# Optimization experiments

Hardware: AMD Instinct MI355X
Metric: run time of the kernel (lower is better)

The kernel has to match this reference:

```python
import jax, jax.numpy as jnp
import numpy as np

B, S, H, DH = 2, 4096, 8, 64
D = H * DH  # 512

def setup_inputs() -> dict:
    key = jax.random.key(0)
    ks = jax.random.split(key, 9)
    sc = 1.0 / np.sqrt(D)
    return {
        "hidden_states": jax.random.normal(ks[0], (B, S, D), jnp.float32),
        "Wq": jax.random.normal(ks[1], (D, D), jnp.float32) * sc,
        "bq": jax.random.normal(ks[2], (D,), jnp.float32) * 0.02,
        "Wk": jax.random.normal(ks[3], (D, D), jnp.float32) * sc,
        "bk": jax.random.normal(ks[4], (D,), jnp.float32) * 0.02,
        "Wv": jax.random.normal(ks[5], (D, D), jnp.float32) * sc,
        "bv": jax.random.normal(ks[6], (D,), jnp.float32) * 0.02,
        "Wo": jax.random.normal(ks[7], (D, D), jnp.float32) * sc,
        "bo": jax.random.normal(ks[8], (D,), jnp.float32) * 0.02,
    }

def _split_heads(t):
    # (B, S, H*DH) -> (B, H, S, DH)
    b = t.shape[0]
    return t.reshape(b, S, H, DH).transpose(0, 2, 1, 3)

def reference(hidden_states, Wq, bq, Wk, bk, Wv, bv, Wo, bo):
    q = _split_heads(hidden_states @ Wq + bq)
    k = _split_heads(hidden_states @ Wk + bk)
    v = _split_heads(hidden_states @ Wv + bv)
    scale = 1.0 / jnp.sqrt(jnp.asarray(DH, q.dtype))
    energy = jnp.einsum('bhqd,bhkd->bhqk', q, k) * scale
    weights = jax.nn.softmax(energy, axis=-1)  # full O(S^2) matrix, as in source
    attended = jnp.einsum('bhqv,bhvd->bhqd', weights, v)
    merged = attended.transpose(0, 2, 1, 3).reshape(hidden_states.shape[0], S, D)
    return merged @ Wo + bo
```

## Files before the change

kernel.cpp:

```cpp
#include <hip/hip_runtime.h>
#include <cstdint>

typedef __bf16 bf16;
typedef __bf16 bf16x4 __attribute__((ext_vector_type(4)));
typedef __bf16 bf16x8 __attribute__((ext_vector_type(8)));
typedef float floatx4 __attribute__((ext_vector_type(4)));

#define MFMA32(a, b, c) __builtin_amdgcn_mfma_f32_16x16x32_bf16((a), (b), (c), 0, 0, 0)

__device__ inline bf16x8 cvt8(const float* p) {
    float4 u = *(const float4*)p;
    float4 v = *(const float4*)(p + 4);
    bf16x8 r;
    r[0] = (bf16)u.x; r[1] = (bf16)u.y; r[2] = (bf16)u.z; r[3] = (bf16)u.w;
    r[4] = (bf16)v.x; r[5] = (bf16)v.y; r[6] = (bf16)v.z; r[7] = (bf16)v.w;
    return r;
}

__global__ __launch_bounds__(256) void k_transpose(
    const float* __restrict__ w0, const float* __restrict__ w1,
    const float* __restrict__ w2, const float* __restrict__ w3,
    bf16* __restrict__ o0, bf16* __restrict__ o1,
    bf16* __restrict__ o2, bf16* __restrict__ o3)
{
    __shared__ float t[32][33];
    const float* in;
    bf16* out;
    switch (blockIdx.z) {
        case 0: in = w0; out = o0; break;
        case 1: in = w1; out = o1; break;
        case 2: in = w2; out = o2; break;
        default: in = w3; out = o3; break;
    }
    const int tx = threadIdx.x & 31;
    const int ty = threadIdx.x >> 5;
    const int r0 = blockIdx.y * 32;
    const int c0 = blockIdx.x * 32;
    #pragma unroll
    for (int i = 0; i < 32; i += 8)
        t[ty + i][tx] = in[(size_t)(r0 + ty + i) * 512 + c0 + tx];
    __syncthreads();
    #pragma unroll
    for (int i = 0; i < 32; i += 8)
        out[(size_t)(c0 + ty + i) * 512 + r0 + tx] = (bf16)t[tx][ty + i];
}

__global__ __launch_bounds__(256) void k_cvtx(
    const float* __restrict__ X, bf16* __restrict__ Xb)
{
    const size_t idx = ((size_t)blockIdx.x * 256 + threadIdx.x) * 8;
    *(bf16x8*)(Xb + idx) = cvt8(X + idx);
}

__global__ __launch_bounds__(256) void k_qkv(
    const bf16* __restrict__ Xb, const bf16* __restrict__ Wcat,
    const float* __restrict__ bq, const float* __restrict__ bk, const float* __restrict__ bv,
    bf16* __restrict__ Qs, bf16* __restrict__ Ks, bf16* __restrict__ Vt)
{
    __shared__ __align__(16) unsigned char smem[36864];
    uint4* Al = (uint4*)smem;
    uint4* Bl = (uint4*)(smem + 16384);

    const int tid  = threadIdx.x;
    const int w    = tid >> 6;
    const int lane = tid & 63;
    const int col  = lane & 15;
    const int quad = lane >> 4;
    const int m0 = blockIdx.x * 128;
    const int n0 = blockIdx.y * 128;

    const bf16* gA0 = Xb   + (size_t)(m0 + (tid >> 2)) * 512 + (tid & 3) * 8;
    const bf16* gA1 = gA0 + 64 * 512;
    const bf16* gB0 = Wcat + (size_t)(n0 + (tid >> 2)) * 512 + (tid & 3) * 8;
    const bf16* gB1 = gB0 + 64 * 512;

    const floatx4 zf = {0.f, 0.f, 0.f, 0.f};
    floatx4 acc[4][4];
    #pragma unroll
    for (int a = 0; a < 4; ++a)
        #pragma unroll
        for (int b = 0; b < 4; ++b) acc[a][b] = zf;

    Al[tid]       = *(const uint4*)gA0;
    Al[tid + 256] = *(const uint4*)gA1;
    Bl[tid]       = *(const uint4*)gB0;
    Bl[tid + 256] = *(const uint4*)gB1;
    __syncthreads();

    const int mb = (w & 1) * 64;
    const int nb = (w >> 1) * 64;

    int buf = 0;
    for (int kk = 0; kk < 16; ++kk) {
        const int kn = ((kk + 1) & 15) * 32;
        const uint4 pa0 = *(const uint4*)(gA0 + kn);
        const uint4 pa1 = *(const uint4*)(gA1 + kn);
        const uint4 pb0 = *(const uint4*)(gB0 + kn);
        const uint4 pb1 = *(const uint4*)(gB1 + kn);

        const uint4* A4 = Al + buf * 512;
        const uint4* B4 = Bl + buf * 512;
        bf16x8 af[4], bfr[4];
        #pragma unroll
        for (int t = 0; t < 4; ++t) {
            union { uint4 u; bf16x8 v; } ca, cb;
            ca.u = A4[(mb + 16 * t + col) * 4 + quad];
            cb.u = B4[(nb + 16 * t + col) * 4 + quad];
            af[t] = ca.v;
            bfr[t] = cb.v;
        }
        #pragma unroll
        for (int tm = 0; tm < 4; ++tm)
            #pragma unroll
            for (int tn = 0; tn < 4; ++tn)
                acc[tm][tn] = MFMA32(af[tm], bfr[tn], acc[tm][tn]);

        const int nbuf = buf ^ 1;
        Al[nbuf * 512 + tid]       = pa0;
        Al[nbuf * 512 + tid + 256] = pa1;
        Bl[nbuf * 512 + tid]       = pb0;
        Bl[nbuf * 512 + tid + 256] = pb1;
        __syncthreads();
        buf = nbuf;
    }

    bf16* ep = (bf16*)smem + (size_t)w * 64 * 72;

    const int which = blockIdx.y >> 2;
    const int nbase = (blockIdx.y & 3) * 128 + nb;
    const int h  = nbase >> 6;
    const int mw = m0 + mb;
    const int b  = mw >> 12;
    const int s0 = mw & 4095;
    const float qsc = 0.125f * 1.44269504088896f;

    if (which == 2) {
        #pragma unroll
        for (int tn = 0; tn < 4; ++tn) {
            const int d = 16 * tn + col;
            const float bb = bv[nbase + d];
            #pragma unroll
            for (int tm = 0; tm < 4; ++tm) {
                union { bf16 e[4]; uint2 u; } pk;
                #pragma unroll
                for (int r = 0; r < 4; ++r) pk.e[r] = (bf16)(acc[tm][tn][r] + bb);
                *(uint2*)(ep + d * 72 + 16 * tm + 4 * quad) = pk.u;
            }
        }
    } else {
        const float* bias = (which == 0) ? bq : bk;
        const float sc = (which == 0) ? qsc : 1.0f;
        #pragma unroll
        for (int tn = 0; tn < 4; ++tn) {
            const int d = 16 * tn + col;
            const float bb = bias[nbase + d];
            #pragma unroll
            for (int tm = 0; tm < 4; ++tm)
                #pragma unroll
                for (int r = 0; r < 4; ++r)
                    ep[(16 * tm + 4 * quad + r) * 72 + d] = (bf16)((acc[tm][tn][r] + bb) * sc);
        }
    }

    asm volatile("" ::: "memory");

    const int rl = lane >> 3;
    const int ch = lane & 7;
    bf16* gbase;
    size_t rowstride;
    if (which == 2) {
        gbase = Vt + (((size_t)b * 8 + h) * 64) * 4096 + s0;
        rowstride = 4096;
    } else {
        bf16* P = (which == 0) ? Qs : Ks;
        gbase = P + (((size_t)b * 8 + h) * 4096 + s0) * 64;
        rowstride = 64;
    }
    #pragma unroll
    for (int it = 0; it < 8; ++it) {
        const int row = it * 8 + rl;
        const uint4 v = *(const uint4*)(ep + row * 72 + ch * 8);
        *(uint4*)(gbase + (size_t)row * rowstride + ch * 8) = v;
    }
}

__global__ __launch_bounds__(512) __attribute__((amdgpu_waves_per_eu(4, 4))) void k_attn(
    const bf16* __restrict__ Qs, const bf16* __restrict__ Ks, const bf16* __restrict__ Vt,
    bf16* __restrict__ att)
{
    __shared__ __align__(16) unsigned char smem[33280];
    uint4* Klds = (uint4*)smem;
    uint4* Vlds = (uint4*)(smem + 16384);
    float* Of   = (float*)smem;
    float* Ls   = (float*)(smem + 32768);

    const int tid  = threadIdx.x;
    const int w    = tid >> 6;
    const int hf   = w >> 2;
    const int wq   = w & 3;
    const int lane = tid & 63;
    const int col  = lane & 15;
    const int quad = lane >> 4;
    const int i    = blockIdx.x;
    const int bh   = ((i & 7) << 1) | ((i >> 3) & 1);
    const int q0   = (i >> 4) * 128 + wq * 32;

    const bf16* Qb = Qs + (size_t)bh * 262144;
    const bf16* Kb = Ks + (size_t)bh * 262144 + (size_t)hf * 2048 * 64;
    const bf16* Vb = Vt + (size_t)bh * 262144 + (size_t)hf * 2048;

    const int t8  = tid & 255;
    const int rK  = t8 >> 3;
    const int lcK = (t8 & 7) ^ (rK & 7);
    const bf16* gK = Kb + (size_t)rK * 64 + lcK * 8;
    const int pV  = t8 >> 3;
    const int ccV = (t8 & 7) ^ (pV & 7);
    const int dV  = 2 * pV + (ccV >> 2);
    const int cV  = ccV & 3;
    const bf16* gV = Vb + (size_t)dV * 4096 + cV * 8;

    uint4* Kl2 = Klds + hf * 512;
    uint4* Vl2 = Vlds + hf * 512;

    bf16x8 aq[2][2];
    #pragma unroll
    for (int s = 0; s < 2; ++s)
        #pragma unroll
        for (int c = 0; c < 2; ++c)
            aq[s][c] = *(const bf16x8*)(Qb + (size_t)(q0 + 16 * s + col) * 64 + 32 * c + quad * 8);

    const floatx4 zf = {0.f, 0.f, 0.f, 0.f};
    floatx4 o[2][4];
    float lsum[2] = {0.f, 0.f};
    #pragma unroll
    for (int s = 0; s < 2; ++s)
        #pragma unroll
        for (int dt = 0; dt < 4; ++dt) o[s][dt] = zf;

    const int c1 = col & 1, ch2 = col >> 1, qh = quad >> 1, ql = quad & 1;

    Kl2[t8] = *(const uint4*)gK;
    Vl2[t8] = *(const uint4*)gV;
    __syncthreads();

    int buf = 0;
    for (int kt = 0; kt < 2048; kt += 32) {
        const int kn = (kt + 32) & 2047;
        const uint4 kreg = *(const uint4*)(gK + (size_t)kn * 64);
        const uint4 vreg = *(const uint4*)(gV + kn);

        const uint4* Kl = Kl2 + buf * 256;
        const uint2* Vl = (const uint2*)(Vl2 + buf * 256);

        bf16x8 kf[2][2];
        #pragma unroll
        for (int t = 0; t < 2; ++t)
            #pragma unroll
            for (int c = 0; c < 2; ++c) {
                union { uint4 u; bf16x8 v; } cv;
                cv.u = Kl[(16 * t + col) * 8 + ((quad + 4 * c) ^ (col & 7))];
                kf[t][c] = cv.v;
            }
        bf16x8 vfrag8[4];
        #pragma unroll
        for (int dt = 0; dt < 4; ++dt) {
            union { uint2 u[2]; bf16x8 v; } cv;
            #pragma unroll
            for (int t = 0; t < 2; ++t) {
                const int slot = (dt * 8 + ch2) * 8 + ((c1 * 4 + 2 * t + qh) ^ ch2);
                cv.u[t] = Vl[slot * 2 + ql];
            }
            vfrag8[dt] = cv.v;
        }

        #pragma unroll
        for (int s = 0; s < 2; ++s) {
            union { bf16 e[8]; bf16x8 v; } pw;
            #pragma unroll
            for (int t = 0; t < 2; ++t) {
                floatx4 sc = MFMA32(kf[t][1], aq[s][1], MFMA32(kf[t][0], aq[s][0], zf));
                const float p0 = __builtin_amdgcn_exp2f(sc[0]);
                const float p1 = __builtin_amdgcn_exp2f(sc[1]);
                const float p2 = __builtin_amdgcn_exp2f(sc[2]);
                const float p3 = __builtin_amdgcn_exp2f(sc[3]);
                lsum[s] += (p0 + p1) + (p2 + p3);
                pw.e[4 * t + 0] = (bf16)p0; pw.e[4 * t + 1] = (bf16)p1;
                pw.e[4 * t + 2] = (bf16)p2; pw.e[4 * t + 3] = (bf16)p3;
            }
            #pragma unroll
            for (int dt = 0; dt < 4; ++dt)
                o[s][dt] = MFMA32(vfrag8[dt], pw.v, o[s][dt]);
        }

        Kl2[(buf ^ 1) * 256 + t8] = kreg;
        Vl2[(buf ^ 1) * 256 + t8] = vreg;
        __syncthreads();
        buf ^= 1;
    }

    float lv[2];
    #pragma unroll
    for (int s = 0; s < 2; ++s) {
        float v = lsum[s];
        v += __shfl_xor(v, 16, 64);
        v += __shfl_xor(v, 32, 64);
        lv[s] = v;
    }

    float* op = Of + ((size_t)(wq * 64 + lane)) * 32;
    if (hf == 1) {
        #pragma unroll
        for (int s = 0; s < 2; ++s)
            #pragma unroll
            for (int dt = 0; dt < 4; ++dt) {
                const int f = s * 4 + dt;
                *(floatx4*)(op + ((f + lane) & 7) * 4) = o[s][dt];
            }
        if (quad == 0) {
            Ls[(wq * 2 + 0) * 16 + col] = lv[0];
            Ls[(wq * 2 + 1) * 16 + col] = lv[1];
        }
    }
    __syncthreads();
    if (hf == 0) {
        float inv[2];
        #pragma unroll
        for (int s = 0; s < 2; ++s)
            inv[s] = 1.0f / (lv[s] + Ls[(wq * 2 + s) * 16 + col]);
        const int b  = bh >> 3;
        const int hh = bh & 7;
        #pragma unroll
        for (int s = 0; s < 2; ++s)
            #pragma unroll
            for (int dt = 0; dt < 4; ++dt) {
                const int f = s * 4 + dt;
                const floatx4 po = *(const floatx4*)(op + ((f + lane) & 7) * 4);
                union { bf16 e[4]; uint2 u; } pk;
                #pragma unroll
                for (int r = 0; r < 4; ++r)
                    pk.e[r] = (bf16)((o[s][dt][r] + po[r]) * inv[s]);
                const size_t row = (size_t)b * 4096 + q0 + 16 * s + col;
                *(uint2*)(att + row * 512 + hh * 64 + 16 * dt + 4 * quad) = pk.u;
            }
    }
}

__global__ __launch_bounds__(256) void k_oproj(
    const bf16* __restrict__ att, const bf16* __restrict__ Wto,
    const float* __restrict__ bo, float* __restrict__ out)
{
    __shared__ uint4 Al[2][512];
    __shared__ uint4 Bl[2][512];

    const int tid  = threadIdx.x;
    const int w    = tid >> 6;
    const int lane = tid & 63;
    const int col  = lane & 15;
    const int quad = lane >> 4;
    const int m0 = blockIdx.x * 128;
    const int n0 = blockIdx.y * 128;

    const bf16* gA0 = att + (size_t)(m0 + (tid >> 2)) * 512 + (tid & 3) * 8;
    const bf16* gA1 = gA0 + 64 * 512;
    const bf16* gB0 = Wto + (size_t)(n0 + (tid >> 2)) * 512 + (tid & 3) * 8;
    const bf16* gB1 = gB0 + 64 * 512;

    const floatx4 zf = {0.f, 0.f, 0.f, 0.f};
    floatx4 acc[4][4];
    #pragma unroll
    for (int a = 0; a < 4; ++a)
        #pragma unroll
        for (int b = 0; b < 4; ++b) acc[a][b] = zf;

    Al[0][tid]       = *(const uint4*)gA0;
    Al[0][tid + 256] = *(const uint4*)gA1;
    Bl[0][tid]       = *(const uint4*)gB0;
    Bl[0][tid + 256] = *(const uint4*)gB1;
    __syncthreads();

    const int mb = (w & 1) * 64;
    const int nb = (w >> 1) * 64;

    int buf = 0;
    for (int kk = 0; kk < 16; ++kk) {
        const int kn = ((kk + 1) & 15) * 32;
        const uint4 pa0 = *(const uint4*)(gA0 + kn);
        const uint4 pa1 = *(const uint4*)(gA1 + kn);
        const uint4 pb0 = *(const uint4*)(gB0 + kn);
        const uint4 pb1 = *(const uint4*)(gB1 + kn);

        const uint4* A4 = Al[buf];
        const uint4* B4 = Bl[buf];
        bf16x8 af[4], bfr[4];
        #pragma unroll
        for (int t = 0; t < 4; ++t) {
            union { uint4 u; bf16x8 v; } ca, cb;
            ca.u = A4[(mb + 16 * t + col) * 4 + quad];
            cb.u = B4[(nb + 16 * t + col) * 4 + quad];
            af[t] = ca.v;
            bfr[t] = cb.v;
        }
        #pragma unroll
        for (int tm = 0; tm < 4; ++tm)
            #pragma unroll
            for (int tn = 0; tn < 4; ++tn)
                acc[tm][tn] = MFMA32(af[tm], bfr[tn], acc[tm][tn]);

        Al[buf ^ 1][tid]       = pa0;
        Al[buf ^ 1][tid + 256] = pa1;
        Bl[buf ^ 1][tid]       = pb0;
        Bl[buf ^ 1][tid + 256] = pb1;
        __syncthreads();
        buf ^= 1;
    }

    #pragma unroll
    for (int tn = 0; tn < 4; ++tn) {
        const int n = n0 + nb + 16 * tn + col;
        const float bb = bo[n];
        #pragma unroll
        for (int tm = 0; tm < 4; ++tm)
            #pragma unroll
            for (int r = 0; r < 4; ++r) {
                const int m = m0 + mb + 16 * tm + quad * 4 + r;
                out[(size_t)m * 512 + n] = acc[tm][tn][r] + bb;
            }
    }
}

extern "C" void kernel_launch(void* const* d_in, const int* in_sizes, int n_in,
                              void* d_out, int out_size, void* d_ws, size_t ws_size,
                              hipStream_t stream)
{
    const float* X  = (const float*)d_in[0];
    const float* Wq = (const float*)d_in[1];
    const float* bq = (const float*)d_in[2];
    const float* Wk = (const float*)d_in[3];
    const float* bk = (const float*)d_in[4];
    const float* Wv = (const float*)d_in[5];
    const float* bv = (const float*)d_in[6];
    const float* Wo = (const float*)d_in[7];
    const float* bo = (const float*)d_in[8];

    bf16* Wtq = (bf16*)d_ws;
    bf16* Wtk = Wtq + 512 * 512;
    bf16* Wtv = Wtk + 512 * 512;
    bf16* Wto = Wtv + 512 * 512;
    bf16* Qs  = Wto + 512 * 512;
    bf16* Ks  = Qs + (size_t)16 * 4096 * 64;
    bf16* Vt  = Ks + (size_t)16 * 4096 * 64;
    bf16* att = Vt + (size_t)16 * 4096 * 64;

    bf16* Xb  = (bf16*)d_out;

    k_transpose<<<dim3(16, 16, 4), 256, 0, stream>>>(Wq, Wk, Wv, Wo, Wtq, Wtk, Wtv, Wto);
    k_cvtx<<<2048, 256, 0, stream>>>(X, Xb);
    k_qkv<<<dim3(64, 12), 256, 0, stream>>>(Xb, Wtq, bq, bk, bv, Qs, Ks, Vt);
    k_attn<<<512, 512, 0, stream>>>(Qs, Ks, Vt, att);
    k_oproj<<<dim3(64, 4), 256, 0, stream>>>(att, Wto, bo, (float*)d_out);
}
```

Measured before the change: 194.6 us.

## Give each attention wave 64 query rows with 256-thread blocks

The attention kernel drops from 8 waves per block (32 queries each) to 4 waves (64 queries each). Each wave now reuses the same K and V fragments loaded from LDS across four query subtiles instead of two, which halves LDS fragment reads per MFMA. Each thread now issues two global loads and two LDS stores per K/V tile, and the cross-half reduction buffer is resized to match. The cost is higher register pressure (more accumulators and Q fragments) and a lower occupancy target of 2 waves per EU, so less latency hiding.

```diff
diff --git a/kernel.cpp b/kernel.cpp
--- a/kernel.cpp
+++ b/kernel.cpp
@@ -184,7 +184,7 @@
     }
 }
 
-__global__ __launch_bounds__(512) __attribute__((amdgpu_waves_per_eu(4, 4))) void k_attn(
+__global__ __launch_bounds__(256) __attribute__((amdgpu_waves_per_eu(2, 2))) void k_attn(
     const bf16* __restrict__ Qs, const bf16* __restrict__ Ks, const bf16* __restrict__ Vt,
     bf16* __restrict__ att)
 {
@@ -196,25 +196,25 @@
 
     const int tid  = threadIdx.x;
     const int w    = tid >> 6;
-    const int hf   = w >> 2;
-    const int wq   = w & 3;
+    const int hf   = w >> 1;
+    const int wq   = w & 1;
     const int lane = tid & 63;
     const int col  = lane & 15;
     const int quad = lane >> 4;
     const int i    = blockIdx.x;
     const int bh   = ((i & 7) << 1) | ((i >> 3) & 1);
-    const int q0   = (i >> 4) * 128 + wq * 32;
+    const int q0   = (i >> 4) * 128 + wq * 64;
 
     const bf16* Qb = Qs + (size_t)bh * 262144;
     const bf16* Kb = Ks + (size_t)bh * 262144 + (size_t)hf * 2048 * 64;
     const bf16* Vb = Vt + (size_t)bh * 262144 + (size_t)hf * 2048;
 
-    const int t8  = tid & 255;
-    const int rK  = t8 >> 3;
-    const int lcK = (t8 & 7) ^ (rK & 7);
+    const int t7  = tid & 127;
+    const int rK  = t7 >> 3;
+    const int lcK = (t7 & 7) ^ (rK & 7);
     const bf16* gK = Kb + (size_t)rK * 64 + lcK * 8;
-    const int pV  = t8 >> 3;
-    const int ccV = (t8 & 7) ^ (pV & 7);
+    const int pV  = t7 >> 3;
+    const int ccV = (t7 & 7) ^ (pV & 7);
     const int dV  = 2 * pV + (ccV >> 2);
     const int cV  = ccV & 3;
     const bf16* gV = Vb + (size_t)dV * 4096 + cV * 8;
@@ -222,32 +222,36 @@
     uint4* Kl2 = Klds + hf * 512;
     uint4* Vl2 = Vlds + hf * 512;
 
-    bf16x8 aq[2][2];
-    #pragma unroll
-    for (int s = 0; s < 2; ++s)
+    bf16x8 aq[4][2];
+    #pragma unroll
+    for (int s = 0; s < 4; ++s)
         #pragma unroll
         for (int c = 0; c < 2; ++c)
             aq[s][c] = *(const bf16x8*)(Qb + (size_t)(q0 + 16 * s + col) * 64 + 32 * c + quad * 8);
 
     const floatx4 zf = {0.f, 0.f, 0.f, 0.f};
-    floatx4 o[2][4];
-    float lsum[2] = {0.f, 0.f};
-    #pragma unroll
-    for (int s = 0; s < 2; ++s)
+    floatx4 o[4][4];
+    float lsum[4] = {0.f, 0.f, 0.f, 0.f};
+    #pragma unroll
+    for (int s = 0; s < 4; ++s)
         #pragma unroll
         for (int dt = 0; dt < 4; ++dt) o[s][dt] = zf;
 
     const int c1 = col & 1, ch2 = col >> 1, qh = quad >> 1, ql = quad & 1;
 
-    Kl2[t8] = *(const uint4*)gK;
-    Vl2[t8] = *(const uint4*)gV;
+    Kl2[t7]       = *(const uint4*)gK;
+    Kl2[t7 + 128] = *(const uint4*)(gK + 1024);
+    Vl2[t7]       = *(const uint4*)gV;
+    Vl2[t7 + 128] = *(const uint4*)(gV + 131072);
     __syncthreads();
 
     int buf = 0;
     for (int kt = 0; kt < 2048; kt += 32) {
         const int kn = (kt + 32) & 2047;
-        const uint4 kreg = *(const uint4*)(gK + (size_t)kn * 64);
-        const uint4 vreg = *(const uint4*)(gV + kn);
+        const uint4 kr0 = *(const uint4*)(gK + (size_t)kn * 64);
+        const uint4 kr1 = *(const uint4*)(gK + (size_t)kn * 64 + 1024);
+        const uint4 vr0 = *(const uint4*)(gV + kn);
+        const uint4 vr1 = *(const uint4*)(gV + kn + 131072);
 
         const uint4* Kl = Kl2 + buf * 256;
         const uint2* Vl = (const uint2*)(Vl2 + buf * 256);
@@ -274,7 +278,7 @@
         }
 
         #pragma unroll
-        for (int s = 0; s < 2; ++s) {
+        for (int s = 0; s < 4; ++s) {
             union { bf16 e[8]; bf16x8 v; } pw;
             #pragma unroll
             for (int t = 0; t < 2; ++t) {
@@ -292,49 +296,52 @@
                 o[s][dt] = MFMA32(vfrag8[dt], pw.v, o[s][dt]);
         }
 
-        Kl2[(buf ^ 1) * 256 + t8] = kreg;
-        Vl2[(buf ^ 1) * 256 + t8] = vreg;
+        Kl2[(buf ^ 1) * 256 + t7]       = kr0;
+        Kl2[(buf ^ 1) * 256 + t7 + 128] = kr1;
+        Vl2[(buf ^ 1) * 256 + t7]       = vr0;
+        Vl2[(buf ^ 1) * 256 + t7 + 128] = vr1;
         __syncthreads();
         buf ^= 1;
     }
 
-    float lv[2];
-    #pragma unroll
-    for (int s = 0; s < 2; ++s) {
+    float lv[4];
+    #pragma unroll
+    for (int s = 0; s < 4; ++s) {
         float v = lsum[s];
         v += __shfl_xor(v, 16, 64);
         v += __shfl_xor(v, 32, 64);
         lv[s] = v;
     }
 
-    float* op = Of + ((size_t)(wq * 64 + lane)) * 32;
+    float* op = Of + ((size_t)(wq * 64 + lane)) * 64;
     if (hf == 1) {
         #pragma unroll
-        for (int s = 0; s < 2; ++s)
+        for (int s = 0; s < 4; ++s)
             #pragma unroll
             for (int dt = 0; dt < 4; ++dt) {
                 const int f = s * 4 + dt;
-                *(floatx4*)(op + ((f + lane) & 7) * 4) = o[s][dt];
+                *(floatx4*)(op + ((f + lane) & 15) * 4) = o[s][dt];
             }
         if (quad == 0) {
-            Ls[(wq * 2 + 0) * 16 + col] = lv[0];
-            Ls[(wq * 2 + 1) * 16 + col] = lv[1];
+            #pragma unroll
+            for (int s = 0; s < 4; ++s)
+                Ls[(wq * 4 + s) * 16 + col] = lv[s];
         }
     }
     __syncthreads();
     if (hf == 0) {
-        float inv[2];
-        #pragma unroll
-        for (int s = 0; s < 2; ++s)
-            inv[s] = 1.0f / (lv[s] + Ls[(wq * 2 + s) * 16 + col]);
+        float inv[4];
+        #pragma unroll
+        for (int s = 0; s < 4; ++s)
+            inv[s] = 1.0f / (lv[s] + Ls[(wq * 4 + s) * 16 + col]);
         const int b  = bh >> 3;
         const int hh = bh & 7;
         #pragma unroll
-        for (int s = 0; s < 2; ++s)
+        for (int s = 0; s < 4; ++s)
             #pragma unroll
             for (int dt = 0; dt < 4; ++dt) {
                 const int f = s * 4 + dt;
-                const floatx4 po = *(const floatx4*)(op + ((f + lane) & 7) * 4);
+                const floatx4 po = *(const floatx4*)(op + ((f + lane) & 15) * 4);
                 union { bf16 e[4]; uint2 u; } pk;
                 #pragma unroll
                 for (int r = 0; r < 4; ++r)
@@ -456,6 +463,6 @@
     k_transpose<<<dim3(16, 16, 4), 256, 0, stream>>>(Wq, Wk, Wv, Wo, Wtq, Wtk, Wtv, Wto);
     k_cvtx<<<2048, 256, 0, stream>>>(X, Xb);
     k_qkv<<<dim3(64, 12), 256, 0, stream>>>(Xb, Wtq, bq, bk, bv, Qs, Ks, Vt);
-    k_attn<<<512, 512, 0, stream>>>(Qs, Ks, Vt, att);
+    k_attn<<<512, 256, 0, stream>>>(Qs, Ks, Vt, att);
     k_oproj<<<dim3(64, 4), 256, 0, stream>>>(att, Wto, bo, (float*)d_out);
 }
```

After: 191.0 us. About the same (-1.9%).
